# Performance work log

Measured on AMD Instinct MI355X. Metric: run time of the kernel, lower is better.

## Reference

```python
import jax, jax.numpy as jnp
import numpy as np

D_IN = 128      # input_dim == input_edge_dim == output_dim
H = 512         # hidden_dim
D_OUT = 128
O = 100000      # num objects
T = 200000      # num triples/edges


def setup_inputs() -> dict:
    key = jax.random.key(0)
    ks = jax.random.split(key, 12)
    def kaiming(k, fan_in, fan_out):
        # kaiming_normal_ for Linear: std = sqrt(2 / fan_in)
        return jax.random.normal(k, (fan_in, fan_out), jnp.float32) * np.sqrt(2.0 / fan_in)
    obj_vecs = jax.random.normal(ks[0], (O, D_IN), jnp.float32)
    pred_vecs = jax.random.normal(ks[1], (T, D_IN), jnp.float32)
    edges = jax.random.randint(ks[2], (T, 2), 0, O, jnp.int64 if jax.config.jax_enable_x64 else jnp.int32)
    # net1: [3*D_IN -> H -> 2*H + D_OUT], ReLU after each layer
    W1 = kaiming(ks[3], 3 * D_IN, H); b1 = jnp.zeros((H,), jnp.float32)
    W2 = kaiming(ks[4], H, 2 * H + D_OUT); b2 = jnp.zeros((2 * H + D_OUT,), jnp.float32)
    # net2: [H -> H -> D_OUT], ReLU after each layer
    W3 = kaiming(ks[5], H, H); b3 = jnp.zeros((H,), jnp.float32)
    W4 = kaiming(ks[6], H, D_OUT); b4 = jnp.zeros((D_OUT,), jnp.float32)
    return {"obj_vecs": obj_vecs, "pred_vecs": pred_vecs, "edges": edges,
            "W1": W1, "b1": b1, "W2": W2, "b2": b2,
            "W3": W3, "b3": b3, "W4": W4, "b4": b4}


def reference(obj_vecs, pred_vecs, edges, W1, b1, W2, b2, W3, b3, W4, b4):
    s_idx = edges[:, 0]
    o_idx = edges[:, 1]
    # gather + concat: (T, 3*D_IN)
    cur_t = jnp.concatenate([obj_vecs[s_idx], pred_vecs, obj_vecs[o_idx]], axis=1)
    # net1 MLP (final_nonlinearity=True -> ReLU after both layers)
    h = jax.nn.relu(cur_t @ W1 + b1)                 # (T, H)
    new_t = jax.nn.relu(h @ W2 + b2)                 # (T, 2H + D_OUT)
    new_s = new_t[:, :H]
    new_p = new_t[:, H:H + D_OUT]
    new_o = new_t[:, H + D_OUT:]
    # scatter-add pooling over object slots
    n_obj = obj_vecs.shape[0]
    pooled = jnp.zeros((n_obj, H), dtype=obj_vecs.dtype)
    pooled = pooled.at[s_idx].add(new_s).at[o_idx].add(new_o)
    # avg pooling: divide by per-object triple count (clamped at 1)
    ones = jnp.ones((new_s.shape[0],), dtype=obj_vecs.dtype)
    counts = jnp.zeros((n_obj,), dtype=obj_vecs.dtype).at[s_idx].add(ones).at[o_idx].add(ones)
    pooled = pooled / jnp.maximum(counts, 1.0)[:, None]
    # net2 MLP
    new_obj = jax.nn.relu(jax.nn.relu(pooled @ W3 + b3) @ W4 + b4)  # (O, D_OUT)
    return new_obj, new_p
```

## Files before the change

kernel.cpp:

```cpp
#include <hip/hip_runtime.h>
#include <hip/hip_bf16.h>
#include <stdint.h>

typedef __bf16 bf16_t;
typedef __attribute__((ext_vector_type(8))) __bf16 bf16x8;
typedef __attribute__((ext_vector_type(4))) __bf16 bf16x4;
typedef __attribute__((ext_vector_type(4))) float f32x4;

#define O_N 100000
#define T_N 200000
#define LDN 136
#define SCB 98

__device__ __forceinline__ bf16x8 cvt8(const float* p) {
    f32x4 a = *(const f32x4*)p;
    f32x4 b = *(const f32x4*)(p + 4);
    bf16x8 v;
    v[0] = (bf16_t)a[0]; v[1] = (bf16_t)a[1]; v[2] = (bf16_t)a[2]; v[3] = (bf16_t)a[3];
    v[4] = (bf16_t)b[0]; v[5] = (bf16_t)b[1]; v[6] = (bf16_t)b[2]; v[7] = (bf16_t)b[3];
    return v;
}

__device__ __forceinline__ void gload16(const bf16_t* g, bf16_t* l) {
    auto gp = reinterpret_cast<const __attribute__((address_space(1))) void*>(
        reinterpret_cast<uintptr_t>(g));
    auto lp = reinterpret_cast<__attribute__((address_space(3))) void*>(
        reinterpret_cast<uintptr_t>(l));
    __builtin_amdgcn_global_load_lds(gp, lp, 16, 0, 0);
}

__device__ __forceinline__ void swz_block(int& mbase, int& nbase) {
    const int gx   = gridDim.x;
    const int nwg  = gx * gridDim.y;
    const int orig = blockIdx.y * gx + blockIdx.x;
    const int q = nwg >> 3, r = nwg & 7;
    const int xcd = orig & 7, lo = orig >> 3;
    const int base = (xcd < r) ? xcd * (q + 1) : r * (q + 1) + (xcd - r) * q;
    const int id = base + lo;
    nbase = (id % gx) * 128;
    mbase = (id / gx) * 128;
}

template<int MODE, int N, int K>
__launch_bounds__(256)
__global__ void gemm_k(const bf16_t* __restrict__ A,
                       const bf16_t* __restrict__ AobjB,
                       const float*  __restrict__ ApredF,
                       const int*    __restrict__ edges,
                       const float*  __restrict__ countsIn,
                       const bf16_t* __restrict__ Bt,
                       const float*  __restrict__ bias,
                       bf16_t*       __restrict__ CoutB,
                       float*        __restrict__ CoutF,
                       int M)
{
    __shared__ bf16_t smem[32768];
    __shared__ int sIdxL[128], oIdxL[128];

    const int tid  = threadIdx.x;
    const int lane = tid & 63;
    const int wv   = tid >> 6;
    const int wr   = (wv >> 1) * 64;
    const int wc   = (wv & 1) * 64;
    const int fr   = lane & 15;
    const int rowb = tid >> 3;
    const int colS = ((tid & 7) ^ (rowb & 7)) << 3;
    int mbase, nbase;
    swz_block(mbase, nbase);

    if constexpr (MODE == 1 || MODE == 5) {
        if (tid < 128) {
            int g = mbase + tid; if (g > M - 1) g = M - 1;
            sIdxL[tid] = edges[2 * g];
            oIdxL[tid] = edges[2 * g + 1];
        }
    }
    __syncthreads();

    f32x4 acc[4][4];
    #pragma unroll
    for (int i = 0; i < 4; i++)
        #pragma unroll
        for (int j = 0; j < 4; j++)
            acc[i][j] = (f32x4){0.f, 0.f, 0.f, 0.f};

    auto stage = [&](int p, int k0) {
        bf16_t* lA = smem + p * 16384;
        bf16_t* lB = lA + 8192;
        if constexpr (MODE == 1) {
            if (k0 < 128 || k0 >= 256) {
                const bool sSeg = (k0 < 128);
                const int  seg0 = sSeg ? k0 : (k0 - 256);
                #pragma unroll
                for (int t = 0; t < 4; ++t) {
                    int row = t * 32 + rowb;
                    int gr  = sSeg ? sIdxL[row] : oIdxL[row];
                    gload16(AobjB + (size_t)gr * 128 + seg0 + colS,
                            &lA[t * 2048 + wv * 512]);
                }
            } else {
                #pragma unroll
                for (int t = 0; t < 4; ++t) {
                    int row  = t * 32 + rowb;
                    int grow = mbase + row; if (grow > M - 1) grow = M - 1;
                    bf16x8 v = cvt8(ApredF + (size_t)grow * 128 + (k0 - 128)
                                    + ((tid & 7) << 3));
                    *(bf16x8*)&lA[t * 2048 + rowb * 64 + colS] = v;
                }
            }
        } else {
            #pragma unroll
            for (int t = 0; t < 4; ++t) {
                int row  = t * 32 + rowb;
                int grow = mbase + row; if (grow > M - 1) grow = M - 1;
                gload16(A + (size_t)grow * K + k0 + colS, &lA[t * 2048 + wv * 512]);
            }
        }
        #pragma unroll
        for (int t = 0; t < 4; ++t) {
            int row = t * 32 + rowb;
            gload16(Bt + (size_t)(nbase + row) * K + k0 + colS,
                    &lB[t * 2048 + wv * 512]);
        }
    };

    const int KT = K / 64;
    stage(0, 0);
    asm volatile("s_waitcnt vmcnt(0) lgkmcnt(0)" ::: "memory");
    __builtin_amdgcn_s_barrier();

    int cur = 0;
    for (int kt = 0; kt < KT; ++kt) {
        if (kt + 1 < KT) stage(cur ^ 1, (kt + 1) * 64);
        const bf16_t* lA = smem + cur * 16384;
        const bf16_t* lB = lA + 8192;
        #pragma unroll
        for (int ks8 = 0; ks8 < 8; ks8 += 4) {
            const int c8 = (ks8 + (lane >> 4)) ^ (lane & 7);
            bf16x8 af[4], bfv[4];
            #pragma unroll
            for (int i = 0; i < 4; i++)
                af[i] = *(const bf16x8*)&lA[(wr + i * 16 + fr) * 64 + (c8 << 3)];
            #pragma unroll
            for (int j = 0; j < 4; j++)
                bfv[j] = *(const bf16x8*)&lB[(wc + j * 16 + fr) * 64 + (c8 << 3)];
            #pragma unroll
            for (int i = 0; i < 4; i++)
                #pragma unroll
                for (int j = 0; j < 4; j++)
                    acc[i][j] = __builtin_amdgcn_mfma_f32_16x16x32_bf16(
                        bfv[j], af[i], acc[i][j], 0, 0, 0);
        }
        asm volatile("s_waitcnt vmcnt(0) lgkmcnt(0)" ::: "memory");
        __builtin_amdgcn_s_barrier();
        cur ^= 1;
    }

    if constexpr (MODE == 4) {
        #pragma unroll
        for (int j = 0; j < 4; j++) {
            int nl = wc + j * 16 + (lane >> 4) * 4;
            f32x4 bv = *(const f32x4*)&bias[nbase + nl];
            #pragma unroll
            for (int i = 0; i < 4; i++) {
                int grow = mbase + wr + i * 16 + fr;
                if (grow >= M) continue;
                float v0 = acc[i][j][0] + bv[0]; v0 = v0 > 0.f ? v0 : 0.f;
                float v1 = acc[i][j][1] + bv[1]; v1 = v1 > 0.f ? v1 : 0.f;
                float v2 = acc[i][j][2] + bv[2]; v2 = v2 > 0.f ? v2 : 0.f;
                float v3 = acc[i][j][3] + bv[3]; v3 = v3 > 0.f ? v3 : 0.f;
                f32x4 o = {v0, v1, v2, v3};
                *(f32x4*)&CoutF[(size_t)grow * 128 + nbase + nl] = o;
            }
        }
    } else {
        const bool isNewp = (MODE == 2 || MODE == 5) && (nbase == 512);
        if (isNewp) {
            #pragma unroll
            for (int j = 0; j < 4; j++) {
                int nl = wc + j * 16 + (lane >> 4) * 4;
                f32x4 bv = *(const f32x4*)&bias[nbase + nl];
                #pragma unroll
                for (int i = 0; i < 4; i++) {
                    int grow = mbase + wr + i * 16 + fr;
                    if (grow >= M) continue;
                    float v0 = acc[i][j][0] + bv[0]; v0 = v0 > 0.f ? v0 : 0.f;
                    float v1 = acc[i][j][1] + bv[1]; v1 = v1 > 0.f ? v1 : 0.f;
                    float v2 = acc[i][j][2] + bv[2]; v2 = v2 > 0.f ? v2 : 0.f;
                    float v3 = acc[i][j][3] + bv[3]; v3 = v3 > 0.f ? v3 : 0.f;
                    f32x4 o = {v0, v1, v2, v3};
                    *(f32x4*)&CoutF[(size_t)grow * 128 + nl] = o;
                }
            }
        } else {
            float rcv[4];
            if constexpr (MODE == 3) {
                #pragma unroll
                for (int i = 0; i < 4; i++) {
                    int grow = mbase + wr + i * 16 + fr;
                    if (grow > M - 1) grow = M - 1;
                    float c = countsIn[grow]; c = c > 1.f ? c : 1.f;
                    rcv[i] = 1.f / c;
                }
            }
            #pragma unroll
            for (int j = 0; j < 4; j++) {
                int nl = wc + j * 16 + (lane >> 4) * 4;
                f32x4 bv = *(const f32x4*)&bias[nbase + nl];
                #pragma unroll
                for (int i = 0; i < 4; i++) {
                    int ml = wr + i * 16 + fr;
                    float s = (MODE == 3) ? rcv[i] : 1.f;
                    float v0 = acc[i][j][0] * s + bv[0]; v0 = v0 > 0.f ? v0 : 0.f;
                    float v1 = acc[i][j][1] * s + bv[1]; v1 = v1 > 0.f ? v1 : 0.f;
                    float v2 = acc[i][j][2] * s + bv[2]; v2 = v2 > 0.f ? v2 : 0.f;
                    float v3 = acc[i][j][3] * s + bv[3]; v3 = v3 > 0.f ? v3 : 0.f;
                    bf16x4 pv;
                    pv[0] = (bf16_t)v0; pv[1] = (bf16_t)v1;
                    pv[2] = (bf16_t)v2; pv[3] = (bf16_t)v3;
                    *(bf16x4*)&smem[ml * LDN + nl] = pv;
                }
            }
            __syncthreads();
            const bool isS = (nbase < 512);
            #pragma unroll
            for (int rr = 0; rr < 8; ++rr) {
                int row  = rr * 16 + (tid >> 4);
                int grow = mbase + row;
                if (grow >= M) continue;
                bf16x8 v = *(const bf16x8*)&smem[row * LDN + (tid & 15) * 8];
                if constexpr (MODE == 1 || MODE == 3) {
                    *(bf16x8*)&CoutB[(size_t)grow * 512 + nbase + (tid & 15) * 8] = v;
                } else if constexpr (MODE == 2) {
                    int cb = isS ? nbase : (nbase - 128);
                    *(bf16x8*)&CoutB[(size_t)grow * 1024 + cb + (tid & 15) * 8] = v;
                } else {
                    int cb2  = isS ? nbase : (nbase - 640);
                    int drow = isS ? sIdxL[row] : oIdxL[row];
                    *(bf16x8*)&CoutB[(size_t)drow * 512 + cb2 + (tid & 15) * 8] = v;
                }
            }
        }
    }
}

__global__ void prep_k(const float* __restrict__ obj, bf16_t* __restrict__ objB,
                       const float* __restrict__ W1, bf16_t* __restrict__ W1t,
                       const float* __restrict__ W2, bf16_t* __restrict__ W2t,
                       const float* __restrict__ W3, bf16_t* __restrict__ W3t,
                       const float* __restrict__ W4, bf16_t* __restrict__ W4t,
                       const int* __restrict__ edges, float* __restrict__ counts) {
    int idx = blockIdx.x * 256 + threadIdx.x;
    if (idx < 1600000) {
        bf16x8 v = cvt8(obj + (size_t)idx * 8);
        *(bf16x8*)(objB + (size_t)idx * 8) = v;
        return;
    }
    idx -= 1600000;
    if (idx < 1114112) {
        const float* in; bf16_t* out; int K, N;
        if (idx < 196608)       { in = W1; out = W1t; K = 384; N = 512;  }
        else if (idx < 786432)  { in = W2; out = W2t; K = 512; N = 1152; idx -= 196608; }
        else if (idx < 1048576) { in = W3; out = W3t; K = 512; N = 512;  idx -= 786432; }
        else                    { in = W4; out = W4t; K = 512; N = 128;  idx -= 1048576; }
        int k = idx / N, n = idx - k * N;
        out[n * K + k] = (bf16_t)in[idx];
        return;
    }
    idx -= 1114112;
    if (idx < T_N) {
        unsafeAtomicAdd(&counts[edges[2 * idx]],     1.f);
        unsafeAtomicAdd(&counts[edges[2 * idx + 1]], 1.f);
    }
}

__launch_bounds__(1024)
__global__ void scan1_k(const float* __restrict__ counts, int* __restrict__ bsum) {
    __shared__ int wsum[16];
    const int tid = threadIdx.x, lane = tid & 63, wv = tid >> 6;
    int i = blockIdx.x * 1024 + tid;
    int v = (i < O_N) ? (int)counts[i] : 0;
    #pragma unroll
    for (int d = 1; d < 64; d <<= 1) v += __shfl_xor(v, d, 64);
    if (lane == 0) wsum[wv] = v;
    __syncthreads();
    if (tid == 0) {
        int s = 0;
        #pragma unroll
        for (int k = 0; k < 16; ++k) s += wsum[k];
        bsum[blockIdx.x] = s;
    }
}

__launch_bounds__(1024)
__global__ void scan23_k(const float* __restrict__ counts, const int* __restrict__ bsum,
                         int* __restrict__ offsets, int* __restrict__ cursor) {
    __shared__ int wsum[16];
    __shared__ int pre2[2];
    const int tid = threadIdx.x, lane = tid & 63, wv = tid >> 6;
    int i = blockIdx.x * 1024 + tid;
    int x = (i < O_N) ? (int)counts[i] : 0;
    int v = x;
    #pragma unroll
    for (int d = 1; d < 64; d <<= 1) {
        int u = __shfl_up(v, d, 64);
        if (lane >= d) v += u;
    }
    if (lane == 63) wsum[wv] = v;
    if (tid < 128) {
        int b = (tid < blockIdx.x) ? bsum[tid] : 0;
        #pragma unroll
        for (int d = 1; d < 64; d <<= 1) b += __shfl_xor(b, d, 64);
        if (lane == 0) pre2[tid >> 6] = b;
    }
    __syncthreads();
    if (tid == 0) {
        int run = pre2[0] + pre2[1];
        #pragma unroll
        for (int k = 0; k < 16; ++k) { int t2 = wsum[k]; wsum[k] = run; run += t2; }
        if (blockIdx.x == SCB - 1) offsets[O_N] = run;
    }
    __syncthreads();
    if (i < O_N) { int e = wsum[wv] + (v - x); offsets[i] = e; cursor[i] = e; }
}

__global__ void fill_k(const int* __restrict__ edges, int* __restrict__ cursor,
                       int* __restrict__ slots, int* __restrict__ sslot2) {
    int t = blockIdx.x * 256 + threadIdx.x;
    if (t < T_N) {
        int s = edges[2 * t], o = edges[2 * t + 1];
        int p = atomicAdd(&cursor[s], 1);
        slots[p] = t << 1;
        int q = atomicAdd(&cursor[o], 1);
        slots[q] = (t << 1) | 1;
        sslot2[2 * t]     = p;
        sslot2[2 * t + 1] = q;
    }
}

__launch_bounds__(256)
__global__ void poolS_k(const bf16_t* __restrict__ poolSrc,
                        const int* __restrict__ offsets,
                        bf16_t* __restrict__ pooledB) {
    const int gw   = (blockIdx.x * 256 + threadIdx.x) >> 6;
    const int lane = threadIdx.x & 63;
    if (gw >= O_N) return;
    const int s0 = offsets[gw], s1 = offsets[gw + 1];
    float acc[8];
    #pragma unroll
    for (int l = 0; l < 8; l++) acc[l] = 0.f;
    int j = s0;
    for (; j + 1 < s1; j += 2) {
        bf16x8 a = *(const bf16x8*)(poolSrc + (size_t)j * 512 + lane * 8);
        bf16x8 b = *(const bf16x8*)(poolSrc + (size_t)(j + 1) * 512 + lane * 8);
        #pragma unroll
        for (int l = 0; l < 8; l++) acc[l] += (float)a[l] + (float)b[l];
    }
    if (j < s1) {
        bf16x8 a = *(const bf16x8*)(poolSrc + (size_t)j * 512 + lane * 8);
        #pragma unroll
        for (int l = 0; l < 8; l++) acc[l] += (float)a[l];
    }
    bf16x8 o;
    #pragma unroll
    for (int l = 0; l < 8; l++) o[l] = (bf16_t)acc[l];
    *(bf16x8*)(pooledB + (size_t)gw * 512 + lane * 8) = o;
}

template<bool FIRST>
__launch_bounds__(256)
__global__ void pool_k(const bf16_t* __restrict__ newT, const int* __restrict__ offsets,
                       const int* __restrict__ slots, bf16_t* __restrict__ pooledB,
                       int tbase, int tcount) {
    const int gw   = (blockIdx.x * 256 + threadIdx.x) >> 6;
    const int lane = threadIdx.x & 63;
    if (gw >= O_N) return;
    const int s0 = offsets[gw], s1 = offsets[gw + 1];
    float acc[8];
    #pragma unroll
    for (int l = 0; l < 8; l++) acc[l] = 0.f;
    for (int base = s0; base < s1; base += 64) {
        int nn = s1 - base; if (nn > 64) nn = 64;
        int myslot = (lane < nn) ? slots[base + lane] : 0;
        for (int j = 0; j < nn; ++j) {
            int sl = __shfl(myslot, j, 64);
            int lt = (sl >> 1) - tbase;
            if ((unsigned)lt >= (unsigned)tcount) continue;
            const bf16_t* p = newT + (size_t)lt * 1024 + (sl & 1) * 512 + lane * 8;
            bf16x8 v = *(const bf16x8*)p;
            #pragma unroll
            for (int l = 0; l < 8; l++) acc[l] += (float)v[l];
        }
    }
    bf16_t* dst = pooledB + (size_t)gw * 512 + lane * 8;
    if constexpr (!FIRST) {
        bf16x8 prev = *(const bf16x8*)dst;
        #pragma unroll
        for (int l = 0; l < 8; l++) acc[l] += (float)prev[l];
    }
    bf16x8 o;
    #pragma unroll
    for (int l = 0; l < 8; l++) o[l] = (bf16_t)acc[l];
    *(bf16x8*)dst = o;
}

extern "C" void kernel_launch(void* const* d_in, const int* in_sizes, int n_in,
                              void* d_out, int out_size, void* d_ws, size_t ws_size,
                              hipStream_t stream) {
    const float* obj  = (const float*)d_in[0];
    const float* pred = (const float*)d_in[1];
    const int*   edges= (const int*)d_in[2];
    const float* W1 = (const float*)d_in[3];
    const float* b1 = (const float*)d_in[4];
    const float* W2 = (const float*)d_in[5];
    const float* b2 = (const float*)d_in[6];
    const float* W3 = (const float*)d_in[7];
    const float* b3 = (const float*)d_in[8];
    const float* W4 = (const float*)d_in[9];
    const float* b4 = (const float*)d_in[10];
    float* out = (float*)d_out;

    char* ws = (char*)d_ws;
    auto AL = [](size_t x) { return (x + 255) & ~(size_t)255; };

    size_t o_pooled = 0;
    size_t o_counts = AL(o_pooled + (size_t)O_N * 512 * 2);
    size_t o_offs   = AL(o_counts + (size_t)O_N * 4);
    size_t o_curs   = AL(o_offs   + (size_t)(O_N + 1) * 4);
    size_t o_bsum   = AL(o_curs   + (size_t)O_N * 4);
    size_t o_slots  = AL(o_bsum   + (size_t)128 * 4);
    size_t o_ss2    = AL(o_slots  + (size_t)2 * T_N * 4);
    size_t o_objB   = AL(o_ss2    + (size_t)2 * T_N * 4);
    size_t o_w1     = AL(o_objB   + (size_t)O_N * 128 * 2);
    size_t o_w2     = AL(o_w1 + (size_t)384 * 512 * 2);
    size_t o_w3     = AL(o_w2 + (size_t)512 * 1152 * 2);
    size_t o_w4     = AL(o_w3 + (size_t)512 * 512 * 2);
    size_t o_chunk  = AL(o_w4 + (size_t)512 * 128 * 2);

    const size_t t3sz   = (size_t)O_N * 1024;
    const size_t psSz   = (size_t)2 * T_N * 512 * 2;

    bool scatter = false;
    int  NCH = 2;
    for (int n : {2, 4, 8}) {
        size_t R = (size_t)T_N / n;
        size_t chunk = AL(R * 1024) + psSz;
        size_t need  = o_chunk + (chunk > t3sz ? chunk : t3sz);
        if (ws_size >= need) { scatter = true; NCH = n; break; }
    }
    if (!scatter) {
        NCH = 8;
        for (int n : {2, 4}) {
            size_t R = (size_t)T_N / n;
            size_t chunk = AL(R * 1024) + R * 2048;
            size_t need  = o_chunk + (chunk > t3sz ? chunk : t3sz);
            if (ws_size >= need) { NCH = n; break; }
        }
    }
    const int R  = T_N / NCH;
    const int MB = (R + 127) / 128;

    bf16_t* pooledB = (bf16_t*)(ws + o_pooled);
    float*  counts  = (float*)(ws + o_counts);
    int*    offs    = (int*)(ws + o_offs);
    int*    curs    = (int*)(ws + o_curs);
    int*    bsum    = (int*)(ws + o_bsum);
    int*    slots   = (int*)(ws + o_slots);
    int*    sslot2  = (int*)(ws + o_ss2);
    bf16_t* objB    = (bf16_t*)(ws + o_objB);
    bf16_t* W1t     = (bf16_t*)(ws + o_w1);
    bf16_t* W2t     = (bf16_t*)(ws + o_w2);
    bf16_t* W3t     = (bf16_t*)(ws + o_w3);
    bf16_t* W4t     = (bf16_t*)(ws + o_w4);
    bf16_t* hbuf    = (bf16_t*)(ws + o_chunk);
    bf16_t* stage2  = (bf16_t*)(ws + o_chunk + AL((size_t)R * 1024));
    bf16_t* t3      = (bf16_t*)(ws + o_chunk);

    hipMemsetAsync(counts, 0, (size_t)O_N * 4, stream);

    prep_k<<<(2914112 + 255) / 256, 256, 0, stream>>>(
        obj, objB, W1, W1t, W2, W2t, W3, W3t, W4, W4t, edges, counts);
    scan1_k<<<SCB, 1024, 0, stream>>>(counts, bsum);
    scan23_k<<<SCB, 1024, 0, stream>>>(counts, bsum, offs, curs);
    fill_k<<<(T_N + 255) / 256, 256, 0, stream>>>(edges, curs, slots, sslot2);

    for (int c = 0; c < NCH; ++c) {
        const int row0 = c * R;
        gemm_k<1, 512, 384><<<dim3(4, MB), 256, 0, stream>>>(
            nullptr, objB, pred + (size_t)row0 * 128, edges + 2 * row0,
            nullptr, W1t, b1, hbuf, nullptr, R);
        if (scatter) {
            gemm_k<5, 1152, 512><<<dim3(9, MB), 256, 0, stream>>>(
                hbuf, nullptr, nullptr, sslot2 + 2 * row0,
                nullptr, W2t, b2, stage2,
                out + (size_t)O_N * 128 + (size_t)row0 * 128, R);
        } else {
            gemm_k<2, 1152, 512><<<dim3(9, MB), 256, 0, stream>>>(
                hbuf, nullptr, nullptr, nullptr,
                nullptr, W2t, b2, stage2,
                out + (size_t)O_N * 128 + (size_t)row0 * 128, R);
            if (c == 0)
                pool_k<true><<<(O_N * 64 + 255) / 256, 256, 0, stream>>>(
                    stage2, offs, slots, pooledB, row0, R);
            else
                pool_k<false><<<(O_N * 64 + 255) / 256, 256, 0, stream>>>(
                    stage2, offs, slots, pooledB, row0, R);
        }
    }
    if (scatter)
        poolS_k<<<(O_N * 64 + 255) / 256, 256, 0, stream>>>(stage2, offs, pooledB);

    gemm_k<3, 512, 512><<<dim3(4, 782), 256, 0, stream>>>(
        pooledB, nullptr, nullptr, nullptr, counts,
        W3t, b3, t3, nullptr, O_N);
    gemm_k<4, 128, 512><<<dim3(1, 782), 256, 0, stream>>>(
        t3, nullptr, nullptr, nullptr, nullptr,
        W4t, b4, nullptr, out, O_N);
}
```

Measured before the change: 998.3 us.

## Alias pooled/hidden buffers to force scatter path and persist poolS warps

Workspace is reorganised so pooledB aliases hbuf and t3 aliases stage2, which lowers the memory needed for the scatter-based pooling path and lets it run with only two chunks. The poolS kernel becomes a persistent-style kernel: a fixed grid of 2048 blocks, each warp handling several objects, with the slot-accumulation loop unrolled by four to keep more loads in flight. The goal is to avoid falling back to the atomic-free gather pool_k path and to cut launch and tail overhead in pooling. Aliasing relies on the buffers' lifetimes not overlapping, and fewer resident warps may reduce latency hiding.

```diff
diff --git a/kernel.cpp b/kernel.cpp
--- a/kernel.cpp
+++ b/kernel.cpp
@@ -341,30 +341,37 @@
 __launch_bounds__(256)
 __global__ void poolS_k(const bf16_t* __restrict__ poolSrc,
                         const int* __restrict__ offsets,
-                        bf16_t* __restrict__ pooledB) {
-    const int gw   = (blockIdx.x * 256 + threadIdx.x) >> 6;
+                        bf16_t* __restrict__ pooledB, int cpw) {
+    const int w    = (blockIdx.x * 256 + threadIdx.x) >> 6;
     const int lane = threadIdx.x & 63;
-    if (gw >= O_N) return;
-    const int s0 = offsets[gw], s1 = offsets[gw + 1];
-    float acc[8];
-    #pragma unroll
-    for (int l = 0; l < 8; l++) acc[l] = 0.f;
-    int j = s0;
-    for (; j + 1 < s1; j += 2) {
-        bf16x8 a = *(const bf16x8*)(poolSrc + (size_t)j * 512 + lane * 8);
-        bf16x8 b = *(const bf16x8*)(poolSrc + (size_t)(j + 1) * 512 + lane * 8);
-        #pragma unroll
-        for (int l = 0; l < 8; l++) acc[l] += (float)a[l] + (float)b[l];
-    }
-    if (j < s1) {
-        bf16x8 a = *(const bf16x8*)(poolSrc + (size_t)j * 512 + lane * 8);
-        #pragma unroll
-        for (int l = 0; l < 8; l++) acc[l] += (float)a[l];
-    }
-    bf16x8 o;
-    #pragma unroll
-    for (int l = 0; l < 8; l++) o[l] = (bf16_t)acc[l];
-    *(bf16x8*)(pooledB + (size_t)gw * 512 + lane * 8) = o;
+    int g0 = w * cpw;
+    int g1 = g0 + cpw; if (g1 > O_N) g1 = O_N;
+    if (g0 >= O_N) return;
+    for (int gw = g0; gw < g1; ++gw) {
+        const int s0 = offsets[gw], s1 = offsets[gw + 1];
+        float acc[8];
+        #pragma unroll
+        for (int l = 0; l < 8; l++) acc[l] = 0.f;
+        int j = s0;
+        for (; j + 3 < s1; j += 4) {
+            bf16x8 a = *(const bf16x8*)(poolSrc + (size_t)j * 512 + lane * 8);
+            bf16x8 b = *(const bf16x8*)(poolSrc + (size_t)(j + 1) * 512 + lane * 8);
+            bf16x8 c = *(const bf16x8*)(poolSrc + (size_t)(j + 2) * 512 + lane * 8);
+            bf16x8 d = *(const bf16x8*)(poolSrc + (size_t)(j + 3) * 512 + lane * 8);
+            #pragma unroll
+            for (int l = 0; l < 8; l++)
+                acc[l] += ((float)a[l] + (float)b[l]) + ((float)c[l] + (float)d[l]);
+        }
+        for (; j < s1; ++j) {
+            bf16x8 a = *(const bf16x8*)(poolSrc + (size_t)j * 512 + lane * 8);
+            #pragma unroll
+            for (int l = 0; l < 8; l++) acc[l] += (float)a[l];
+        }
+        bf16x8 o;
+        #pragma unroll
+        for (int l = 0; l < 8; l++) o[l] = (bf16_t)acc[l];
+        *(bf16x8*)(pooledB + (size_t)gw * 512 + lane * 8) = o;
+    }
 }
 
 template<bool FIRST>
@@ -423,8 +430,7 @@
     char* ws = (char*)d_ws;
     auto AL = [](size_t x) { return (x + 255) & ~(size_t)255; };
 
-    size_t o_pooled = 0;
-    size_t o_counts = AL(o_pooled + (size_t)O_N * 512 * 2);
+    size_t o_counts = 0;
     size_t o_offs   = AL(o_counts + (size_t)O_N * 4);
     size_t o_curs   = AL(o_offs   + (size_t)(O_N + 1) * 4);
     size_t o_bsum   = AL(o_curs   + (size_t)O_N * 4);
@@ -435,32 +441,31 @@
     size_t o_w2     = AL(o_w1 + (size_t)384 * 512 * 2);
     size_t o_w3     = AL(o_w2 + (size_t)512 * 1152 * 2);
     size_t o_w4     = AL(o_w3 + (size_t)512 * 512 * 2);
-    size_t o_chunk  = AL(o_w4 + (size_t)512 * 128 * 2);
-
-    const size_t t3sz   = (size_t)O_N * 1024;
-    const size_t psSz   = (size_t)2 * T_N * 512 * 2;
+    size_t o_end    = AL(o_w4 + (size_t)512 * 128 * 2);
+
+    const size_t pbSz = (size_t)O_N * 512 * 2;
+    const size_t psSz = (size_t)2 * T_N * 512 * 2;
+    const size_t t3sz = (size_t)O_N * 512 * 2;
 
     bool scatter = false;
     int  NCH = 2;
-    for (int n : {2, 4, 8}) {
-        size_t R = (size_t)T_N / n;
-        size_t chunk = AL(R * 1024) + psSz;
-        size_t need  = o_chunk + (chunk > t3sz ? chunk : t3sz);
-        if (ws_size >= need) { scatter = true; NCH = n; break; }
+    {
+        size_t hb = (size_t)(T_N / 2) * 1024; if (hb < pbSz) hb = pbSz;
+        size_t need = o_end + AL(hb) + psSz;
+        if (ws_size >= need) scatter = true;
     }
     if (!scatter) {
         NCH = 8;
         for (int n : {2, 4}) {
             size_t R = (size_t)T_N / n;
             size_t chunk = AL(R * 1024) + R * 2048;
-            size_t need  = o_chunk + (chunk > t3sz ? chunk : t3sz);
+            size_t need  = o_end + AL(pbSz) + (chunk > t3sz ? chunk : t3sz);
             if (ws_size >= need) { NCH = n; break; }
         }
     }
     const int R  = T_N / NCH;
     const int MB = (R + 127) / 128;
 
-    bf16_t* pooledB = (bf16_t*)(ws + o_pooled);
     float*  counts  = (float*)(ws + o_counts);
     int*    offs    = (int*)(ws + o_offs);
     int*    curs    = (int*)(ws + o_curs);
@@ -472,9 +477,20 @@
     bf16_t* W2t     = (bf16_t*)(ws + o_w2);
     bf16_t* W3t     = (bf16_t*)(ws + o_w3);
     bf16_t* W4t     = (bf16_t*)(ws + o_w4);
-    bf16_t* hbuf    = (bf16_t*)(ws + o_chunk);
-    bf16_t* stage2  = (bf16_t*)(ws + o_chunk + AL((size_t)R * 1024));
-    bf16_t* t3      = (bf16_t*)(ws + o_chunk);
+
+    bf16_t *hbuf, *pooledB, *stage2, *t3;
+    if (scatter) {
+        size_t hb = (size_t)R * 1024; if (hb < pbSz) hb = pbSz;
+        hbuf    = (bf16_t*)(ws + o_end);
+        pooledB = hbuf;
+        stage2  = (bf16_t*)(ws + o_end + AL(hb));
+        t3      = stage2;
+    } else {
+        pooledB = (bf16_t*)(ws + o_end);
+        hbuf    = (bf16_t*)(ws + o_end + AL(pbSz));
+        stage2  = (bf16_t*)((char*)hbuf + AL((size_t)R * 1024));
+        t3      = hbuf;
+    }
 
     hipMemsetAsync(counts, 0, (size_t)O_N * 4, stream);
 
@@ -507,8 +523,11 @@
                     stage2, offs, slots, pooledB, row0, R);
         }
     }
-    if (scatter)
-        poolS_k<<<(O_N * 64 + 255) / 256, 256, 0, stream>>>(stage2, offs, pooledB);
+    if (scatter) {
+        const int NBLK = 2048;
+        const int cpw  = (O_N + NBLK * 4 - 1) / (NBLK * 4);
+        poolS_k<<<NBLK, 256, 0, stream>>>(stage2, offs, pooledB, cpw);
+    }
 
     gemm_k<3, 512, 512><<<dim3(4, 782), 256, 0, stream>>>(
         pooledB, nullptr, nullptr, nullptr, counts,
```

Result: slower. 1.041 ms (+4.3%).
